# Performance work log

Measured on AMD Instinct MI355X. Metric: run time of the kernel, lower is better.

## Reference

```python
import jax, jax.numpy as jnp
import numpy as np

D_MODEL = 1024
H = 16
D_K = D_MODEL // H


def setup_inputs() -> dict:
    key = jax.random.key(0)
    ks = jax.random.split(key, 7)
    B, S = 4, 2048
    scale = 1.0 / np.sqrt(D_MODEL)
    return {
        "q": jax.random.normal(ks[0], (B, S, D_MODEL), dtype=jnp.float32),
        "k": jax.random.normal(ks[1], (B, S, D_MODEL), dtype=jnp.float32),
        "v": jax.random.normal(ks[2], (B, S, D_MODEL), dtype=jnp.float32),
        "W_q": jax.random.normal(ks[3], (D_MODEL, D_MODEL), dtype=jnp.float32) * scale,
        "W_k": jax.random.normal(ks[4], (D_MODEL, D_MODEL), dtype=jnp.float32) * scale,
        "W_v": jax.random.normal(ks[5], (D_MODEL, D_MODEL), dtype=jnp.float32) * scale,
        "W_o": jax.random.normal(ks[6], (D_MODEL, D_MODEL), dtype=jnp.float32) * scale,
    }


def reference(q, k, v, W_q, W_k, W_v, W_o):
    B, S, _ = q.shape
    # nn.Linear(bias=False): y = x @ W.T
    def proj(x, W):
        return (x @ W.T).reshape(B, -1, H, D_K).transpose(0, 2, 1, 3)  # [B,H,S,d_k]
    Q = proj(q, W_q)
    K = proj(k, W_k)
    V = proj(v, W_v)
    scores = jnp.einsum('bhqd,bhkd->bhqk', Q, K) / jnp.sqrt(jnp.float32(D_K))
    attn = jax.nn.softmax(scores, axis=-1)  # dropout p=0.0 -> identity
    ctx = jnp.einsum('bhqk,bhkd->bhqd', attn, V)
    ctx = ctx.transpose(0, 2, 1, 3).reshape(B, S, H * D_K)
    return ctx @ W_o.T
```

## Files before the change

kernel.cpp:

```cpp
#include <hip/hip_runtime.h>
#include <stdint.h>


typedef __attribute__((ext_vector_type(8))) short bf16x8;
typedef __attribute__((ext_vector_type(4))) float f32x4;

__device__ __forceinline__ void lds_async16(const void* g, void* l) {
  __builtin_amdgcn_global_load_lds(
      (const __attribute__((address_space(1))) void*)g,
      (__attribute__((address_space(3))) void*)l, 16, 0, 0);
}

__device__ __forceinline__ unsigned short f2bf(float f) {
  union { float f; unsigned u; } v; v.f = f;
  unsigned u = v.u + 0x7fffu + ((v.u >> 16) & 1u);
  return (unsigned short)(u >> 16);
}

__device__ __forceinline__ float fast_exp2(float x) {
#if __has_builtin(__builtin_amdgcn_exp2f)
  return __builtin_amdgcn_exp2f(x);
#else
  return exp2f(x);
#endif
}

__device__ __forceinline__ uint2 pack4(float a, float b, float c, float d) {
#if __has_builtin(__builtin_amdgcn_cvt_pk_bf16_f32)
  typedef __bf16 bf16v2 __attribute__((ext_vector_type(2)));
  union U { bf16v2 v; unsigned u; };
  U x, y;
  x.v = __builtin_amdgcn_cvt_pk_bf16_f32(a, b);
  y.v = __builtin_amdgcn_cvt_pk_bf16_f32(c, d);
  return make_uint2(x.u, y.u);
#else
  return make_uint2((unsigned)f2bf(a) | ((unsigned)f2bf(b) << 16),
                    (unsigned)f2bf(c) | ((unsigned)f2bf(d) << 16));
#endif
}

__global__ void cvt_kernel(const float* s0, const float* s1, const float* s2, const float* s3,
                           unsigned short* d0, unsigned short* d1, unsigned short* d2, unsigned short* d3,
                           int n4) {
  int which = blockIdx.y;
  const float* s = which == 0 ? s0 : which == 1 ? s1 : which == 2 ? s2 : s3;
  unsigned short* d = which == 0 ? d0 : which == 1 ? d1 : which == 2 ? d2 : d3;
  int i = blockIdx.x * 256 + threadIdx.x;
  if (i < n4) {
    float4 v = ((const float4*)s)[i];
    ushort4 o;
    o.x = f2bf(v.x); o.y = f2bf(v.y); o.z = f2bf(v.z); o.w = f2bf(v.w);
    ((ushort4*)d)[i] = o;
  }
}

struct GemmAcc { f32x4 acc[4][4]; };

__device__ __forceinline__ void gemm_core(const unsigned short* __restrict__ Arows,
                                          const unsigned short* __restrict__ Brows,
                                          int tm, int tn, unsigned short* As,
                                          unsigned short* Bs, GemmAcc& g) {
  constexpr int K = 1024;
  const int tid = threadIdx.x;
  const int lane = tid & 63;
  const int wv = tid >> 6;
  const int wm = wv & 1, wn = wv >> 1;
  const int c16 = lane & 15, q4 = lane >> 4;

#pragma unroll
  for (int i = 0; i < 4; ++i)
#pragma unroll
    for (int j = 0; j < 4; ++j)
#pragma unroll
      for (int r = 0; r < 4; ++r) g.acc[i][j][r] = 0.f;

  const int srow = tid >> 3;
  const int gc = (((tid & 7) ^ (srow & 7)) << 3);
  const unsigned short* Arow = Arows + (size_t)(tm * 128 + srow) * K + gc;
  const unsigned short* Brow = Brows + (size_t)(tn * 128 + srow) * K + gc;
  char* AsBase = (char*)As + tid * 16;
  char* BsBase = (char*)Bs + tid * 16;

  for (int k0 = 0; k0 < K; k0 += 64) {
    __syncthreads();
#pragma unroll
    for (int i = 0; i < 4; ++i) {
      lds_async16(Arow + k0 + i * 32 * K, AsBase + i * 4096);
      lds_async16(Brow + k0 + i * 32 * K, BsBase + i * 4096);
    }
    __syncthreads();
#pragma unroll
    for (int ks = 0; ks < 2; ++ks) {
      bf16x8 af[4], bfr[4];
#pragma unroll
      for (int i = 0; i < 4; ++i) {
        int mr = wm * 64 + i * 16 + c16;
        int pa = (ks * 4 + q4) ^ (mr & 7);
        af[i] = *(const bf16x8*)(As + mr * 64 + pa * 8);
        int nr = wn * 64 + i * 16 + c16;
        int pb = (ks * 4 + q4) ^ (nr & 7);
        bfr[i] = *(const bf16x8*)(Bs + nr * 64 + pb * 8);
      }
#pragma unroll
      for (int i = 0; i < 4; ++i)
#pragma unroll
        for (int j = 0; j < 4; ++j)
          g.acc[i][j] = __builtin_amdgcn_mfma_f32_16x16x32_bf16(af[i], bfr[j], g.acc[i][j], 0, 0, 0);
    }
  }
}

__global__ __launch_bounds__(256, 2)
void qkv_kernel(const unsigned short* __restrict__ qb, const unsigned short* __restrict__ kb,
                const unsigned short* __restrict__ vb,
                const unsigned short* __restrict__ wq, const unsigned short* __restrict__ wk,
                const unsigned short* __restrict__ wv_,
                unsigned short* __restrict__ Qb, unsigned short* __restrict__ Kb,
                unsigned short* __restrict__ Vtb) {
  __shared__ unsigned short As[128 * 64];
  __shared__ unsigned short Bs[128 * 64];
  const int z = blockIdx.z;
  const unsigned short* A;
  const unsigned short* B;
  int tm, tn;
  if (z == 0)      { A = qb;  B = wq;  tm = blockIdx.y; tn = blockIdx.x; }
  else if (z == 1) { A = kb;  B = wk;  tm = blockIdx.y; tn = blockIdx.x; }
  else             { A = wv_; B = vb;  tm = blockIdx.x; tn = blockIdx.y; }

  GemmAcc g;
  gemm_core(A, B, tm, tn, As, Bs, g);

  const int lane = threadIdx.x & 63;
  const int wv = threadIdx.x >> 6;
  const int wm = wv & 1, wn = wv >> 1;
  const int c16 = lane & 15, q4 = lane >> 4;
  const float qscale = 0.125f * 1.44269504f;

#pragma unroll
  for (int i = 0; i < 4; ++i)
#pragma unroll
    for (int j = 0; j < 4; ++j)
#pragma unroll
      for (int r = 0; r < 4; ++r) {
        int m = tm * 128 + wm * 64 + i * 16 + q4 * 4 + r;
        int n = tn * 128 + wn * 64 + j * 16 + c16;
        float val = g.acc[i][j][r];
        if (z < 2) {
          if (z == 0) val *= qscale;
          int b = m >> 11, s_ = m & 2047, h = n >> 6, d = n & 63;
          unsigned short* dst = z == 0 ? Qb : Kb;
          dst[(((size_t)(b * 16 + h) * 2048 + s_) << 6) | d] = f2bf(val);
        } else {
          int h = m >> 6, d = m & 63, b = n >> 11, s_ = n & 2047;
          Vtb[((size_t)((b * 16 + h) * 64 + d) << 11) | s_] = f2bf(val);
        }
      }
}

__global__ __launch_bounds__(256, 2)
void out_gemm(const unsigned short* __restrict__ A, const unsigned short* __restrict__ B,
              float* __restrict__ C) {
  __shared__ unsigned short As[128 * 64];
  __shared__ unsigned short Bs[128 * 64];
  GemmAcc g;
  gemm_core(A, B, blockIdx.y, blockIdx.x, As, Bs, g);
  const int lane = threadIdx.x & 63;
  const int wv = threadIdx.x >> 6;
  const int wm = wv & 1, wn = wv >> 1;
  const int c16 = lane & 15, q4 = lane >> 4;
#pragma unroll
  for (int i = 0; i < 4; ++i)
#pragma unroll
    for (int j = 0; j < 4; ++j)
#pragma unroll
      for (int r = 0; r < 4; ++r) {
        int m = blockIdx.y * 128 + wm * 64 + i * 16 + q4 * 4 + r;
        int n = blockIdx.x * 128 + wn * 64 + j * 16 + c16;
        C[(size_t)m * 1024 + n] = g.acc[i][j][r];
      }
}

__global__ __launch_bounds__(256, 2)
void attn_kernel(const unsigned short* __restrict__ Q,
                 const unsigned short* __restrict__ K,
                 const unsigned short* __restrict__ Vt,
                 unsigned short* __restrict__ ctx) {
  __shared__ unsigned short Ks[128 * 64];
  __shared__ unsigned short Vs[64 * 128];
  __shared__ unsigned short Ps[128 * 128];

  const int tid = threadIdx.x, lane = tid & 63, w = tid >> 6;
  const int c16 = lane & 15, q4 = lane >> 4;
  const int wbase = w * 32;
  const int bh = blockIdx.y, qt = blockIdx.x;
  const unsigned short* Qp = Q + ((size_t)bh * 2048 + qt * 128) * 64;
  const unsigned short* Kp = K + (size_t)bh * 2048 * 64;
  const unsigned short* Vp = Vt + (size_t)bh * 64 * 2048;

  const int srow8 = tid >> 3;
  const int gc8 = (((tid & 7) ^ (srow8 & 7)) << 3);

  {
    const unsigned short* Qr = Qp + (size_t)srow8 * 64 + gc8;
    char* base = (char*)Ps + tid * 16;
#pragma unroll
    for (int c = 0; c < 4; ++c) lds_async16(Qr + c * 32 * 64, base + c * 4096);
  }
  __syncthreads();
  bf16x8 qf[2][2];
#pragma unroll
  for (int nn = 0; nn < 2; ++nn)
#pragma unroll
    for (int ks = 0; ks < 2; ++ks) {
      int qr = wbase + nn * 16 + c16;
      int pos = (ks * 4 + q4) ^ (qr & 7);
      qf[nn][ks] = *(const bf16x8*)(Ps + qr * 64 + pos * 8);
    }

  bf16x8 onesf;
  {
    short v = (c16 == 0) ? (short)0x3F80 : (short)0;
#pragma unroll
    for (int j = 0; j < 8; ++j) onesf[j] = v;
  }

  f32x4 oacc[2][4];
  f32x4 lacc[2];
#pragma unroll
  for (int mm = 0; mm < 2; ++mm) {
#pragma unroll
    for (int r = 0; r < 4; ++r) lacc[mm][r] = 0.f;
#pragma unroll
    for (int dj = 0; dj < 4; ++dj)
#pragma unroll
      for (int r = 0; r < 4; ++r) oacc[mm][dj][r] = 0.f;
  }

  const int vrow = tid >> 4;
  const int vslot = tid & 15;
  const int vchunk = vslot ^ (vrow & 15);

  const int ckbase = (q4 >> 1);
  const int ckoff = (q4 & 1) * 4;

  for (int kt = 0; kt < 16; ++kt) {
    __syncthreads();
    {
      const unsigned short* Kr = Kp + ((size_t)kt * 128 + srow8) * 64 + gc8;
      char* base = (char*)Ks + tid * 16;
#pragma unroll
      for (int c = 0; c < 4; ++c) lds_async16(Kr + c * 32 * 64, base + c * 4096);
    }
    {
      const unsigned short* Vr = Vp + (size_t)vrow * 2048 + kt * 128 + vchunk * 8;
      char* base = (char*)Vs + tid * 16;
#pragma unroll
      for (int c = 0; c < 4; ++c) lds_async16(Vr + (size_t)c * 16 * 2048, base + c * 4096);
    }
    __syncthreads();

#pragma unroll
    for (int m = 0; m < 8; ++m) {
      bf16x8 kf0, kf1;
      {
        int row = m * 16 + c16;
        kf0 = *(const bf16x8*)(Ks + row * 64 + ((0 + q4) ^ (row & 7)) * 8);
        kf1 = *(const bf16x8*)(Ks + row * 64 + ((4 + q4) ^ (row & 7)) * 8);
      }
      f32x4 s0 = {0.f, 0.f, 0.f, 0.f}, s1 = {0.f, 0.f, 0.f, 0.f};
      s0 = __builtin_amdgcn_mfma_f32_16x16x32_bf16(kf0, qf[0][0], s0, 0, 0, 0);
      s0 = __builtin_amdgcn_mfma_f32_16x16x32_bf16(kf1, qf[0][1], s0, 0, 0, 0);
      s1 = __builtin_amdgcn_mfma_f32_16x16x32_bf16(kf0, qf[1][0], s1, 0, 0, 0);
      s1 = __builtin_amdgcn_mfma_f32_16x16x32_bf16(kf1, qf[1][1], s1, 0, 0, 0);
      int ck = m * 2 + ckbase;
      {
        int q = wbase + c16;
        int pos = ck ^ ((q & 7) ^ ((q & 8) >> 2));
        *(uint2*)(Ps + q * 128 + pos * 8 + ckoff) =
            pack4(fast_exp2(s0[0]), fast_exp2(s0[1]), fast_exp2(s0[2]), fast_exp2(s0[3]));
      }
      {
        int q = wbase + 16 + c16;
        int pos = ck ^ ((q & 7) ^ ((q & 8) >> 2));
        *(uint2*)(Ps + q * 128 + pos * 8 + ckoff) =
            pack4(fast_exp2(s1[0]), fast_exp2(s1[1]), fast_exp2(s1[2]), fast_exp2(s1[3]));
      }
    }

#pragma unroll
    for (int ks2 = 0; ks2 < 4; ++ks2) {
      bf16x8 vf[4];
#pragma unroll
      for (int dj = 0; dj < 4; ++dj) {
        int dr = dj * 16 + c16;
        int pos = (ks2 * 4 + q4) ^ (dr & 15);
        vf[dj] = *(const bf16x8*)(Vs + dr * 128 + pos * 8);
      }
      bf16x8 pf[2];
#pragma unroll
      for (int mm = 0; mm < 2; ++mm) {
        int qr = wbase + mm * 16 + c16;
        int pos = (ks2 * 4 + q4) ^ ((qr & 7) ^ ((qr & 8) >> 2));
        pf[mm] = *(const bf16x8*)(Ps + qr * 128 + pos * 8);
      }
#pragma unroll
      for (int mm = 0; mm < 2; ++mm) {
        lacc[mm] = __builtin_amdgcn_mfma_f32_16x16x32_bf16(pf[mm], onesf, lacc[mm], 0, 0, 0);
#pragma unroll
        for (int dj = 0; dj < 4; ++dj)
          oacc[mm][dj] = __builtin_amdgcn_mfma_f32_16x16x32_bf16(pf[mm], vf[dj], oacc[mm][dj], 0, 0, 0);
      }
    }
  }

  int b = bh >> 4, h = bh & 15;
#pragma unroll
  for (int mm = 0; mm < 2; ++mm)
#pragma unroll
    for (int r = 0; r < 4; ++r) {
      float l = __shfl(lacc[mm][r], lane & 48, 64);
      float inv = 1.f / l;
      int s_ = qt * 128 + wbase + mm * 16 + q4 * 4 + r;
#pragma unroll
      for (int dj = 0; dj < 4; ++dj) {
        int d = dj * 16 + c16;
        ctx[((size_t)(b * 2048 + s_)) * 1024 + h * 64 + d] = f2bf(oacc[mm][dj][r] * inv);
      }
    }
}

extern "C" void kernel_launch(void* const* d_in, const int* in_sizes, int n_in,
                              void* d_out, int out_size, void* d_ws, size_t ws_size,
                              hipStream_t stream) {
  const float* q  = (const float*)d_in[0];
  const float* k  = (const float*)d_in[1];
  const float* v  = (const float*)d_in[2];
  const float* Wq = (const float*)d_in[3];
  const float* Wk = (const float*)d_in[4];
  const float* Wv = (const float*)d_in[5];
  const float* Wo = (const float*)d_in[6];

  char* ws = (char*)d_ws;
  unsigned short* qb  = (unsigned short*)(ws);
  unsigned short* kb  = (unsigned short*)(ws + (16u << 20));
  unsigned short* vb  = (unsigned short*)(ws + (32u << 20));
  unsigned short* wqb = (unsigned short*)(ws + (48u << 20));
  unsigned short* wkb = (unsigned short*)(ws + (50u << 20));
  unsigned short* wvb = (unsigned short*)(ws + (52u << 20));
  unsigned short* wob = (unsigned short*)(ws + (54u << 20));
  unsigned short* Qb  = (unsigned short*)(ws + (56u << 20));
  unsigned short* Kb  = (unsigned short*)(ws + (72u << 20));
  unsigned short* Vtb = (unsigned short*)(ws + (88u << 20));
  unsigned short* ctxb = qb;

  cvt_kernel<<<dim3(1024, 4), 256, 0, stream>>>(Wq, Wk, Wv, Wo, wqb, wkb, wvb, wob, 262144);
  cvt_kernel<<<dim3(8192, 3), 256, 0, stream>>>(q, k, v, q, qb, kb, vb, qb, 2097152);

  qkv_kernel<<<dim3(8, 64, 3), 256, 0, stream>>>(qb, kb, vb, wqb, wkb, wvb, Qb, Kb, Vtb);

  attn_kernel<<<dim3(16, 64), 256, 0, stream>>>(Qb, Kb, Vtb, ctxb);

  out_gemm<<<dim3(8, 64), 256, 0, stream>>>(ctxb, wob, (float*)d_out);
}
```

Measured before the change: 342.8 us.

## Keep attention probabilities in registers instead of staging through LDS

The exp'd score tile no longer goes through a 32 KB LDS buffer. The S=K·Q MFMA output is packed straight into bf16 A-operand fragments, and V is read with a matching permuted k-order (two 8-byte LDS reads per fragment) so the PV MFMA lines up without a write/read round-trip. This drops LDS traffic, cuts LDS footprint from 64 KB to 32 KB, and raises launch bounds to 4 blocks per CU for more occupancy. In exchange there are more, smaller LDS reads of V, and register pressure under the tighter launch bound may cause spills.

```diff
diff --git a/kernel.cpp b/kernel.cpp
--- a/kernel.cpp
+++ b/kernel.cpp
@@ -3,6 +3,7 @@
 
 
 typedef __attribute__((ext_vector_type(8))) short bf16x8;
+typedef __attribute__((ext_vector_type(4))) short bf16x4;
 typedef __attribute__((ext_vector_type(4))) float f32x4;
 
 __device__ __forceinline__ void lds_async16(const void* g, void* l) {
@@ -25,17 +26,14 @@
 #endif
 }
 
-__device__ __forceinline__ uint2 pack4(float a, float b, float c, float d) {
+__device__ __forceinline__ unsigned pk2(float a, float b) {
 #if __has_builtin(__builtin_amdgcn_cvt_pk_bf16_f32)
   typedef __bf16 bf16v2 __attribute__((ext_vector_type(2)));
-  union U { bf16v2 v; unsigned u; };
-  U x, y;
+  union { bf16v2 v; unsigned u; } x;
   x.v = __builtin_amdgcn_cvt_pk_bf16_f32(a, b);
-  y.v = __builtin_amdgcn_cvt_pk_bf16_f32(c, d);
-  return make_uint2(x.u, y.u);
+  return x.u;
 #else
-  return make_uint2((unsigned)f2bf(a) | ((unsigned)f2bf(b) << 16),
-                    (unsigned)f2bf(c) | ((unsigned)f2bf(d) << 16));
+  return (unsigned)f2bf(a) | ((unsigned)f2bf(b) << 16);
 #endif
 }
 
@@ -180,14 +178,13 @@
       }
 }
 
-__global__ __launch_bounds__(256, 2)
+__global__ __launch_bounds__(256, 4)
 void attn_kernel(const unsigned short* __restrict__ Q,
                  const unsigned short* __restrict__ K,
                  const unsigned short* __restrict__ Vt,
                  unsigned short* __restrict__ ctx) {
   __shared__ unsigned short Ks[128 * 64];
   __shared__ unsigned short Vs[64 * 128];
-  __shared__ unsigned short Ps[128 * 128];
 
   const int tid = threadIdx.x, lane = tid & 63, w = tid >> 6;
   const int c16 = lane & 15, q4 = lane >> 4;
@@ -202,7 +199,7 @@
 
   {
     const unsigned short* Qr = Qp + (size_t)srow8 * 64 + gc8;
-    char* base = (char*)Ps + tid * 16;
+    char* base = (char*)Ks + tid * 16;
 #pragma unroll
     for (int c = 0; c < 4; ++c) lds_async16(Qr + c * 32 * 64, base + c * 4096);
   }
@@ -214,7 +211,7 @@
     for (int ks = 0; ks < 2; ++ks) {
       int qr = wbase + nn * 16 + c16;
       int pos = (ks * 4 + q4) ^ (qr & 7);
-      qf[nn][ks] = *(const bf16x8*)(Ps + qr * 64 + pos * 8);
+      qf[nn][ks] = *(const bf16x8*)(Ks + qr * 64 + pos * 8);
     }
 
   bf16x8 onesf;
@@ -239,9 +236,6 @@
   const int vrow = tid >> 4;
   const int vslot = tid & 15;
   const int vchunk = vslot ^ (vrow & 15);
-
-  const int ckbase = (q4 >> 1);
-  const int ckoff = (q4 & 1) * 4;
 
   for (int kt = 0; kt < 16; ++kt) {
     __syncthreads();
@@ -260,55 +254,42 @@
     __syncthreads();
 
 #pragma unroll
-    for (int m = 0; m < 8; ++m) {
-      bf16x8 kf0, kf1;
-      {
-        int row = m * 16 + c16;
-        kf0 = *(const bf16x8*)(Ks + row * 64 + ((0 + q4) ^ (row & 7)) * 8);
-        kf1 = *(const bf16x8*)(Ks + row * 64 + ((4 + q4) ^ (row & 7)) * 8);
-      }
-      f32x4 s0 = {0.f, 0.f, 0.f, 0.f}, s1 = {0.f, 0.f, 0.f, 0.f};
-      s0 = __builtin_amdgcn_mfma_f32_16x16x32_bf16(kf0, qf[0][0], s0, 0, 0, 0);
-      s0 = __builtin_amdgcn_mfma_f32_16x16x32_bf16(kf1, qf[0][1], s0, 0, 0, 0);
-      s1 = __builtin_amdgcn_mfma_f32_16x16x32_bf16(kf0, qf[1][0], s1, 0, 0, 0);
-      s1 = __builtin_amdgcn_mfma_f32_16x16x32_bf16(kf1, qf[1][1], s1, 0, 0, 0);
-      int ck = m * 2 + ckbase;
-      {
-        int q = wbase + c16;
-        int pos = ck ^ ((q & 7) ^ ((q & 8) >> 2));
-        *(uint2*)(Ps + q * 128 + pos * 8 + ckoff) =
-            pack4(fast_exp2(s0[0]), fast_exp2(s0[1]), fast_exp2(s0[2]), fast_exp2(s0[3]));
-      }
-      {
-        int q = wbase + 16 + c16;
-        int pos = ck ^ ((q & 7) ^ ((q & 8) >> 2));
-        *(uint2*)(Ps + q * 128 + pos * 8 + ckoff) =
-            pack4(fast_exp2(s1[0]), fast_exp2(s1[1]), fast_exp2(s1[2]), fast_exp2(s1[3]));
-      }
-    }
-
-#pragma unroll
     for (int ks2 = 0; ks2 < 4; ++ks2) {
-      bf16x8 vf[4];
+      f32x4 s[2][2];
+#pragma unroll
+      for (int ms = 0; ms < 2; ++ms) {
+        const int row = (ks2 * 2 + ms) * 16 + c16;
+        const bf16x8 kf0 = *(const bf16x8*)(Ks + row * 64 + ((0 + q4) ^ (row & 7)) * 8);
+        const bf16x8 kf1 = *(const bf16x8*)(Ks + row * 64 + ((4 + q4) ^ (row & 7)) * 8);
+        f32x4 z0 = {0.f, 0.f, 0.f, 0.f}, z1 = {0.f, 0.f, 0.f, 0.f};
+        z0 = __builtin_amdgcn_mfma_f32_16x16x32_bf16(kf0, qf[0][0], z0, 0, 0, 0);
+        z0 = __builtin_amdgcn_mfma_f32_16x16x32_bf16(kf1, qf[0][1], z0, 0, 0, 0);
+        z1 = __builtin_amdgcn_mfma_f32_16x16x32_bf16(kf0, qf[1][0], z1, 0, 0, 0);
+        z1 = __builtin_amdgcn_mfma_f32_16x16x32_bf16(kf1, qf[1][1], z1, 0, 0, 0);
+        s[ms][0] = z0;
+        s[ms][1] = z1;
+      }
+      union PU { unsigned u[4]; bf16x8 v; };
+      PU pf0, pf1;
+#pragma unroll
+      for (int ms = 0; ms < 2; ++ms) {
+        pf0.u[ms * 2]     = pk2(fast_exp2(s[ms][0][0]), fast_exp2(s[ms][0][1]));
+        pf0.u[ms * 2 + 1] = pk2(fast_exp2(s[ms][0][2]), fast_exp2(s[ms][0][3]));
+        pf1.u[ms * 2]     = pk2(fast_exp2(s[ms][1][0]), fast_exp2(s[ms][1][1]));
+        pf1.u[ms * 2 + 1] = pk2(fast_exp2(s[ms][1][2]), fast_exp2(s[ms][1][3]));
+      }
+      lacc[0] = __builtin_amdgcn_mfma_f32_16x16x32_bf16(pf0.v, onesf, lacc[0], 0, 0, 0);
+      lacc[1] = __builtin_amdgcn_mfma_f32_16x16x32_bf16(pf1.v, onesf, lacc[1], 0, 0, 0);
+      const int cb = ks2 * 4 + (q4 >> 1);
+      const int co = (q4 & 1) * 4;
 #pragma unroll
       for (int dj = 0; dj < 4; ++dj) {
-        int dr = dj * 16 + c16;
-        int pos = (ks2 * 4 + q4) ^ (dr & 15);
-        vf[dj] = *(const bf16x8*)(Vs + dr * 128 + pos * 8);
-      }
-      bf16x8 pf[2];
-#pragma unroll
-      for (int mm = 0; mm < 2; ++mm) {
-        int qr = wbase + mm * 16 + c16;
-        int pos = (ks2 * 4 + q4) ^ ((qr & 7) ^ ((qr & 8) >> 2));
-        pf[mm] = *(const bf16x8*)(Ps + qr * 128 + pos * 8);
-      }
-#pragma unroll
-      for (int mm = 0; mm < 2; ++mm) {
-        lacc[mm] = __builtin_amdgcn_mfma_f32_16x16x32_bf16(pf[mm], onesf, lacc[mm], 0, 0, 0);
-#pragma unroll
-        for (int dj = 0; dj < 4; ++dj)
-          oacc[mm][dj] = __builtin_amdgcn_mfma_f32_16x16x32_bf16(pf[mm], vf[dj], oacc[mm][dj], 0, 0, 0);
+        const int dr = dj * 16 + c16;
+        union VU { bf16x4 h[2]; bf16x8 v; } vf;
+        vf.h[0] = *(const bf16x4*)(Vs + dr * 128 + ((cb) ^ (dr & 15)) * 8 + co);
+        vf.h[1] = *(const bf16x4*)(Vs + dr * 128 + ((cb + 2) ^ (dr & 15)) * 8 + co);
+        oacc[0][dj] = __builtin_amdgcn_mfma_f32_16x16x32_bf16(pf0.v, vf.v, oacc[0][dj], 0, 0, 0);
+        oacc[1][dj] = __builtin_amdgcn_mfma_f32_16x16x32_bf16(pf1.v, vf.v, oacc[1][dj], 0, 0, 0);
       }
     }
   }
```

New measurement: 329.4 us. -3.9%, faster.
